# Kernel optimization log

Hardware: AMD Instinct MI355X
Metric: run time of the kernel (lower is better)

Reference implementation:

```python
import jax, jax.numpy as jnp
import numpy as np

EPS = 1e-5
HEADS, DK, DV, FMAP = 8, 32, 64, 32


def _bn(x, gamma, beta, mean, var):
    # inference-mode BatchNorm2d over channel dim of (b, c, h, w)
    inv = gamma / jnp.sqrt(var + EPS)
    return x * inv[None, :, None, None] + (beta - mean * inv)[None, :, None, None]


def setup_inputs() -> dict:
    key = jax.random.key(0)
    ks = jax.random.split(key, 24)
    B, C = 8, 256
    idk, idv = DK * HEADS, DV * HEADS  # 256, 512
    inp = {}
    inp['x'] = jax.random.normal(ks[0], (B, C, FMAP, FMAP), jnp.float32)
    inp['wq'] = jax.random.normal(ks[1], (idk, C), jnp.float32) * (C ** -0.5)
    inp['qgam'] = jax.random.uniform(ks[2], (idk,), jnp.float32, 0.5, 1.5)
    inp['qbet'] = jax.random.normal(ks[3], (idk,), jnp.float32) * 0.1
    inp['qmu'] = jax.random.normal(ks[4], (idk,), jnp.float32) * 0.1
    inp['qvar'] = jax.random.uniform(ks[5], (idk,), jnp.float32, 0.5, 1.5)
    inp['wk'] = jax.random.normal(ks[6], (idk, C), jnp.float32) * (C ** -0.5)
    inp['kgam'] = jax.random.uniform(ks[7], (idk,), jnp.float32, 0.5, 1.5)
    inp['kbet'] = jax.random.normal(ks[8], (idk,), jnp.float32) * 0.1
    inp['kmu'] = jax.random.normal(ks[9], (idk,), jnp.float32) * 0.1
    inp['kvar'] = jax.random.uniform(ks[10], (idk,), jnp.float32, 0.5, 1.5)
    inp['wv'] = jax.random.normal(ks[11], (idv, C), jnp.float32) * (C ** -0.5)
    inp['vgam'] = jax.random.uniform(ks[12], (idv,), jnp.float32, 0.5, 1.5)
    inp['vbet'] = jax.random.normal(ks[13], (idv,), jnp.float32) * 0.1
    inp['vmu'] = jax.random.normal(ks[14], (idv,), jnp.float32) * 0.1
    inp['vvar'] = jax.random.uniform(ks[15], (idv,), jnp.float32, 0.5, 1.5)
    inp['wo'] = jax.random.normal(ks[16], (C, idv), jnp.float32) * (idv ** -0.5)
    inp['bo'] = jax.random.normal(ks[17], (C,), jnp.float32) * 0.1
    inp['ogam'] = jax.random.uniform(ks[18], (C,), jnp.float32, 0.5, 1.5)
    inp['obet'] = jax.random.normal(ks[19], (C,), jnp.float32) * 0.1
    inp['omu'] = jax.random.normal(ks[20], (C,), jnp.float32) * 0.1
    inp['ovar'] = jax.random.uniform(ks[21], (C,), jnp.float32, 0.5, 1.5)
    inp['pos_emb'] = jax.random.normal(ks[22], (FMAP * FMAP, HEADS), jnp.float32) * 0.02
    # deterministic relative-position index buffer, exactly as in the module
    r = np.arange(FMAP)
    pos = np.stack(np.meshgrid(r, r, indexing='ij'), axis=-1).reshape(-1, 2)  # (n, 2)
    rel = np.abs(pos[:, None, :] - pos[None, :, :])  # (n, n, 2)
    inp['pos_indices'] = jnp.asarray(rel[..., 0] * FMAP + rel[..., 1], jnp.int32)
    return inp


def reference(x, wq, qgam, qbet, qmu, qvar, wk, kgam, kbet, kmu, kvar,
              wv, vgam, vbet, vmu, vvar, wo, bo, ogam, obet, omu, ovar,
              pos_emb, pos_indices):
    scale = DK ** -0.5
    B = x.shape[0]
    Fh = Fw = FMAP
    n = Fh * Fw

    def proj(w, g, be, m, v):
        y = jnp.einsum('oc,bchw->bohw', w, x)  # 1x1 conv, no bias
        return _bn(y, g, be, m, v)

    q = proj(wq, qgam, qbet, qmu, qvar)   # (b, H*DK, F, F)
    k = proj(wk, kgam, kbet, kmu, kvar)   # (b, H*DK, F, F)
    v = proj(wv, vgam, vbet, vmu, vvar)   # (b, H*DV, F, F)

    # b (h d) x y -> b h n d
    q = q.reshape(B, HEADS, DK, n).transpose(0, 1, 3, 2)
    k = k.reshape(B, HEADS, DK, n).transpose(0, 1, 3, 2)
    v = v.reshape(B, HEADS, DV, n).transpose(0, 1, 3, 2)

    dots = jnp.einsum('bhid,bhjd->bhij', q, k) * scale  # (b, h, n, n)
    bias = pos_emb[pos_indices]                          # (n, n, h)
    dots = dots + bias.transpose(2, 0, 1)[None] / scale

    attn = jax.nn.softmax(dots, axis=-1)
    out = jnp.einsum('bhij,bhjd->bhid', attn, v)         # (b, h, n, DV)
    out = out.transpose(0, 1, 3, 2).reshape(B, HEADS * DV, Fh, Fw)

    out = jax.nn.gelu(out, approximate=False)
    out = jnp.einsum('oc,bchw->bohw', wo, out) + bo[None, :, None, None]
    return _bn(out, ogam, obet, omu, ovar)
```

## Files before the change

kernel.cpp:

```cpp
#include <hip/hip_runtime.h>
#include <math.h>

#define NB 8
#define NHEADS 8
#define NDK 32
#define NDV 64
#define NSEQ 1024
#define NCIN 256

typedef __attribute__((ext_vector_type(8))) short bf16x8;
typedef __attribute__((ext_vector_type(4))) float f32x4;
typedef __attribute__((ext_vector_type(16))) float f32x16;

#define MFMA16(A, B, C) __builtin_amdgcn_mfma_f32_16x16x32_bf16(A, B, C, 0, 0, 0)
#define MFMA32(A, B, C) __builtin_amdgcn_mfma_f32_32x32x16_bf16(A, B, C, 0, 0, 0)

#define SC2 0.2550347873f
#define PE2 8.1611156f

__device__ __forceinline__ short f2bf(float f) {
    union { float f; unsigned u; } v; v.f = f;
    unsigned r = v.u + 0x7FFFu + ((v.u >> 16) & 1u);
    return (short)(r >> 16);
}

__device__ __forceinline__ unsigned cvt_pk_bf16(float lo, float hi) {
    unsigned r;
    asm("v_cvt_pk_bf16_f32 %0, %1, %2" : "=v"(r) : "v"(lo), "v"(hi));
    return r;
}

__device__ __forceinline__ void gload16(const short* g, short* l) {
    __builtin_amdgcn_global_load_lds(
        (const __attribute__((address_space(1))) void*)g,
        (__attribute__((address_space(3))) void*)l, 16, 0, 0);
}

__global__ __launch_bounds__(256) void prep_trans_kernel(
    const float* __restrict__ x, short* __restrict__ Xt,
    const float* __restrict__ wq, const float* __restrict__ qg, const float* __restrict__ qb,
    const float* __restrict__ qm, const float* __restrict__ qv,
    const float* __restrict__ wk, const float* __restrict__ kg, const float* __restrict__ kb,
    const float* __restrict__ km, const float* __restrict__ kv,
    const float* __restrict__ wv, const float* __restrict__ vg, const float* __restrict__ vb,
    const float* __restrict__ vm, const float* __restrict__ vv,
    const float* __restrict__ wo,
    short* __restrict__ Wqkv, float* __restrict__ Bqkv, short* __restrict__ Wo)
{
    __shared__ float tile[64][65];
    int bid = blockIdx.x, t = threadIdx.x;
    if (bid < 512) {
        int p0 = (bid & 15) * 64, c0 = ((bid >> 4) & 3) * 64, b = bid >> 6;
        int tp = t & 63, tr = t >> 6;
        const float* xb = x + ((size_t)b * NCIN + c0) * NSEQ + p0;
#pragma unroll
        for (int i = 0; i < 16; ++i) {
            int cl = tr * 16 + i;
            tile[cl][tp] = xb[(size_t)cl * NSEQ + tp];
        }
        __syncthreads();
        short* xt = Xt + ((size_t)b * NSEQ + p0) * NCIN + c0;
#pragma unroll
        for (int i = 0; i < 16; ++i) {
            int pl = tr * 16 + i;
            xt[(size_t)pl * NCIN + tp] = f2bf(tile[tp][pl]);
        }
    } else {
        int row = bid - 512;
        if (row < 1024) {
            const float *w, *g, *be, *mu, *va; int o; float sc;
            if (row < 256)      { w = wq; o = row;       g = qg; be = qb; mu = qm; va = qv; sc = SC2; }
            else if (row < 512) { w = wk; o = row - 256; g = kg; be = kb; mu = km; va = kv; sc = 1.f; }
            else                { w = wv; o = row - 512; g = vg; be = vb; mu = vm; va = vv; sc = 1.f; }
            float inv = g[o] * rsqrtf(va[o] + 1e-5f) * sc;
            Wqkv[row * NCIN + t] = f2bf(w[o * NCIN + t] * inv);
            if (t == 0) Bqkv[row] = (be[o] - mu[o] * (g[o] * rsqrtf(va[o] + 1e-5f))) * sc;
        } else {
            int o = row - 1024;
            Wo[o * 512 + t]       = f2bf(wo[o * 512 + t]);
            Wo[o * 512 + 256 + t] = f2bf(wo[o * 512 + 256 + t]);
        }
    }
}

__global__ __launch_bounds__(256) void qkv_gemm(
    const short* __restrict__ Xt, const short* __restrict__ Wqkv, const float* __restrict__ Bqkv,
    short* __restrict__ Qo, short* __restrict__ Ko, short* __restrict__ Vto)
{
    __shared__ short At[128][32];
    __shared__ short Bt[128][32];
    int b = blockIdx.z, p0 = blockIdx.x * 128, o0 = blockIdx.y * 128;
    int t = threadIdx.x, wave = t >> 6, lane = t & 63;
    int wr = wave >> 1, wc = wave & 1, lr = lane & 15, lg = lane >> 4;

    const short* Abase = Xt + ((size_t)b * NSEQ + p0) * NCIN;
    const short* Bbase = Wqkv + (size_t)o0 * NCIN;

    int srow = lane >> 2, scol = (lane & 3) * 8;
    int r0 = (wave * 2) * 16 + srow, r1 = (wave * 2 + 1) * 16 + srow;
    short* lA0 = &At[0][0] + (wave * 2) * 512;
    short* lA1 = &At[0][0] + (wave * 2 + 1) * 512;
    short* lB0 = &Bt[0][0] + (wave * 2) * 512;
    short* lB1 = &Bt[0][0] + (wave * 2 + 1) * 512;

    f32x4 acc[4][4];
#pragma unroll
    for (int m = 0; m < 4; ++m)
#pragma unroll
        for (int n = 0; n < 4; ++n) acc[m][n] = (f32x4){0.f, 0.f, 0.f, 0.f};

    for (int k0 = 0; k0 < NCIN; k0 += 32) {
        gload16(Abase + (size_t)r0 * NCIN + k0 + scol, lA0);
        gload16(Abase + (size_t)r1 * NCIN + k0 + scol, lA1);
        gload16(Bbase + (size_t)r0 * NCIN + k0 + scol, lB0);
        gload16(Bbase + (size_t)r1 * NCIN + k0 + scol, lB1);
        __syncthreads();
        bf16x8 af[4], bfr[4];
#pragma unroll
        for (int m = 0; m < 4; ++m) af[m] = *(const bf16x8*)&At[wr * 64 + m * 16 + lr][lg * 8];
#pragma unroll
        for (int n = 0; n < 4; ++n) bfr[n] = *(const bf16x8*)&Bt[wc * 64 + n * 16 + lr][lg * 8];
#pragma unroll
        for (int m = 0; m < 4; ++m)
#pragma unroll
            for (int n = 0; n < 4; ++n)
                acc[m][n] = MFMA16(af[m], bfr[n], acc[m][n]);
        __syncthreads();
    }

#pragma unroll
    for (int n = 0; n < 4; ++n) {
        int o = o0 + wc * 64 + n * 16 + lr;
        float bias = Bqkv[o];
#pragma unroll
        for (int m = 0; m < 4; ++m) {
            int pr = p0 + wr * 64 + m * 16 + lg * 4;
#pragma unroll
            for (int r = 0; r < 4; ++r) {
                float y = acc[m][n][r] + bias;
                short vv = f2bf(y);
                int p = pr + r;
                if (o < 256) {
                    int hh = o >> 5, d = o & 31;
                    Qo[(((size_t)b * NHEADS + hh) * NSEQ + p) * NDK + d] = vv;
                } else if (o < 512) {
                    int oo = o - 256, hh = oo >> 5, d = oo & 31;
                    Ko[(((size_t)b * NHEADS + hh) * NSEQ + p) * NDK + d] = vv;
                } else {
                    int oo = o - 512, hh = oo >> 6, d = oo & 63;
                    Vto[(((size_t)b * NHEADS + hh) * NDV + d) * NSEQ + p] = vv;
                }
            }
        }
    }
}

__global__ __launch_bounds__(256) void attn_kernel(
    const short* __restrict__ Q, const short* __restrict__ K, const short* __restrict__ Vt,
    const float* __restrict__ pos_emb, short* __restrict__ Xg)
{
    __shared__ float peR[32][64];
    __shared__ short Klds[2][64][36];
    __shared__ short Vlds[2][64][68];
    __shared__ short tb[4][32][68];

    int bid = blockIdx.x;
    int h = bid & 7;
    int qt = (bid >> 3) & 7;
    int b = bid >> 6;
    int t = threadIdx.x, wave = t >> 6, l = t & 63, ql = l & 31, hi = l >> 5;

    {
        int dr = t >> 3, y0 = (t & 7) * 8;
#pragma unroll
        for (int k = 0; k < 8; ++k) {
            int y = y0 + k;
            if (y < 63) {
                int d = 31 - y; d = d < 0 ? -d : d;
                peR[dr][y] = pos_emb[(dr * 32 + d) * NHEADS + h] * PE2;
            }
        }
    }

    size_t bh = (size_t)b * NHEADS + h;
    const short* Qb = Q + bh * NSEQ * NDK;
    const short* Kb = K + bh * NSEQ * NDK;
    const short* Vb = Vt + bh * NDV * NSEQ;

    int q0 = qt * 128 + wave * 32;
    int iq = q0 + ql;
    int qr = iq >> 5;
    int pebase = 31 - ql + 4 * hi;

    bf16x8 qf0 = *(const bf16x8*)(Qb + (size_t)iq * NDK + hi * 8);
    bf16x8 qf1 = *(const bf16x8*)(Qb + (size_t)iq * NDK + 16 + hi * 8);

    int krow = t >> 2, kcol = (t & 3) * 8;
    int vrow = t >> 3, vcol = (t & 7) * 8;

    {
        int4 kreg  = *(const int4*)(Kb + (size_t)krow * NDK + kcol);
        int4 vreg0 = *(const int4*)(Vb + (size_t)vrow * NSEQ + vcol);
        int4 vreg1 = *(const int4*)(Vb + (size_t)(vrow + 32) * NSEQ + vcol);
        *(int4*)&Klds[0][krow][kcol] = kreg;
        *(int4*)&Vlds[0][vrow][vcol] = vreg0;
        *(int4*)&Vlds[0][vrow + 32][vcol] = vreg1;
    }
    __syncthreads();

    float lsum = 0.f;
    f32x16 O0, O1;
#pragma unroll
    for (int r = 0; r < 16; ++r) { O0[r] = 0.f; O1[r] = 0.f; }

    int cur = 0;
    for (int jt = 0; jt < 16; ++jt) {
        int4 kreg, vreg0, vreg1;
        if (jt < 15) {
            int j0n = (jt + 1) * 64;
            kreg  = *(const int4*)(Kb + (size_t)(j0n + krow) * NDK + kcol);
            vreg0 = *(const int4*)(Vb + (size_t)vrow * NSEQ + j0n + vcol);
            vreg1 = *(const int4*)(Vb + (size_t)(vrow + 32) * NSEQ + j0n + vcol);
        }

#pragma unroll
        for (int s = 0; s < 2; ++s) {
            int jr = (jt * 64 + s * 32) >> 5;
            int drb = qr - jr; drb = drb < 0 ? -drb : drb;
            const float* per = &peR[drb][pebase];

            bf16x8 kf0 = *(const bf16x8*)&Klds[cur][s * 32 + ql][hi * 8];
            bf16x8 kf1 = *(const bf16x8*)&Klds[cur][s * 32 + ql][16 + hi * 8];

            f32x16 S;
#pragma unroll
            for (int a = 0; a < 4; ++a)
#pragma unroll
                for (int u = 0; u < 4; ++u)
                    S[4 * a + u] = per[8 * a + u];
            S = MFMA32(kf0, qf0, S);
            S = MFMA32(kf1, qf1, S);

            bf16x8 vf[4];
#pragma unroll
            for (int dn = 0; dn < 2; ++dn)
#pragma unroll
                for (int ks = 0; ks < 2; ++ks)
                    vf[dn * 2 + ks] = *(const bf16x8*)&Vlds[cur][dn * 32 + ql][s * 32 + ks * 16 + hi * 8];

#pragma unroll
            for (int r = 0; r < 16; ++r) S[r] = __builtin_amdgcn_exp2f(S[r]);

            {
                float a0 = S[0] + S[1],   a1 = S[2] + S[3];
                float a2 = S[4] + S[5],   a3 = S[6] + S[7];
                float a4 = S[8] + S[9],   a5 = S[10] + S[11];
                float a6 = S[12] + S[13], a7 = S[14] + S[15];
                float b0 = a0 + a1, b1 = a2 + a3, b2 = a4 + a5, b3 = a6 + a7;
                lsum += (b0 + b1) + (b2 + b3);
            }

            unsigned pk[4][2];
#pragma unroll
            for (int a = 0; a < 4; ++a)
#pragma unroll
                for (int u = 0; u < 2; ++u)
                    pk[a][u] = cvt_pk_bf16(S[4 * a + 2 * u], S[4 * a + 2 * u + 1]);

#pragma unroll
            for (int ks = 0; ks < 2; ++ks) {
                unsigned u0 = pk[2 * ks][0], u2 = pk[2 * ks + 1][0];
                unsigned u1 = pk[2 * ks][1], u3 = pk[2 * ks + 1][1];
                asm("v_permlane32_swap_b32 %0, %1" : "+v"(u0), "+v"(u2));
                asm("v_permlane32_swap_b32 %0, %1" : "+v"(u1), "+v"(u3));
                union { bf16x8 v; unsigned u[4]; } pf;
                pf.u[0] = u0; pf.u[1] = u1; pf.u[2] = u2; pf.u[3] = u3;
                O0 = MFMA32(vf[ks], pf.v, O0);
                O1 = MFMA32(vf[2 + ks], pf.v, O1);
            }
        }

        if (jt < 15) {
            *(int4*)&Klds[cur ^ 1][krow][kcol] = kreg;
            *(int4*)&Vlds[cur ^ 1][vrow][vcol] = vreg0;
            *(int4*)&Vlds[cur ^ 1][vrow + 32][vcol] = vreg1;
            __syncthreads();
            cur ^= 1;
        }
    }

    lsum += __shfl_xor(lsum, 32);
    float inv = 1.0f / lsum;

    short (*tw)[68] = tb[wave];
#pragma unroll
    for (int dn = 0; dn < 2; ++dn)
#pragma unroll
        for (int a = 0; a < 4; ++a) {
            short4 w;
#pragma unroll
            for (int bb = 0; bb < 4; ++bb) {
                float v = (dn ? O1[4 * a + bb] : O0[4 * a + bb]) * inv;
                v = 0.5f * v * (1.f + erff(v * 0.70710678118654752f));
                ((short*)&w)[bb] = f2bf(v);
            }
            *(short4*)&tw[ql][dn * 32 + 8 * a + 4 * hi] = w;
        }
#pragma unroll
    for (int c = 0; c < 4; ++c) {
        int4 val = *(const int4*)&tw[ql][(hi * 4 + c) * 8];
        *(int4*)(Xg + ((size_t)b * NSEQ + q0 + ql) * 512 + h * 64 + (hi * 4 + c) * 8) = val;
    }
}

__global__ __launch_bounds__(256) void out_gemm(
    const short* __restrict__ Xg, const short* __restrict__ Wo,
    const float* __restrict__ bo, const float* __restrict__ og, const float* __restrict__ ob,
    const float* __restrict__ om, const float* __restrict__ ov,
    float* __restrict__ out)
{
    __shared__ short At[128][32];
    __shared__ short Bt[64][32];
    int mt = blockIdx.x, nt = blockIdx.y;
    int t = threadIdx.x, wave = t >> 6, lane = t & 63;
    int wr = wave >> 1, wc = wave & 1, lr = lane & 15, lg = lane >> 4;
    int row0 = mt * 128, o0 = nt * 64;

    int srow = lane >> 2, scol = (lane & 3) * 8;
    int rA0 = (wave * 2) * 16 + srow, rA1 = (wave * 2 + 1) * 16 + srow;
    int rB  = wave * 16 + srow;
    short* lA0 = &At[0][0] + (wave * 2) * 512;
    short* lA1 = &At[0][0] + (wave * 2 + 1) * 512;
    short* lB  = &Bt[0][0] + wave * 512;

    f32x4 acc[4][2];
#pragma unroll
    for (int m = 0; m < 4; ++m)
#pragma unroll
        for (int n = 0; n < 2; ++n) acc[m][n] = (f32x4){0.f, 0.f, 0.f, 0.f};

    for (int k0 = 0; k0 < 512; k0 += 32) {
        gload16(Xg + (size_t)(row0 + rA0) * 512 + k0 + scol, lA0);
        gload16(Xg + (size_t)(row0 + rA1) * 512 + k0 + scol, lA1);
        gload16(Wo + (size_t)(o0 + rB) * 512 + k0 + scol, lB);
        __syncthreads();
        bf16x8 af[4], bfr[2];
#pragma unroll
        for (int m = 0; m < 4; ++m) af[m] = *(const bf16x8*)&At[wr * 64 + m * 16 + lr][lg * 8];
#pragma unroll
        for (int n = 0; n < 2; ++n) bfr[n] = *(const bf16x8*)&Bt[wc * 32 + n * 16 + lr][lg * 8];
#pragma unroll
        for (int m = 0; m < 4; ++m)
#pragma unroll
            for (int n = 0; n < 2; ++n)
                acc[m][n] = MFMA16(af[m], bfr[n], acc[m][n]);
        __syncthreads();
    }

    int b = row0 >> 10;
    int pbase = row0 & 1023;
#pragma unroll
    for (int n = 0; n < 2; ++n) {
        int o = o0 + wc * 32 + n * 16 + lr;
        float inv = og[o] * rsqrtf(ov[o] + 1e-5f);
        float off = bo[o] * inv + ob[o] - om[o] * inv;
        float* dst = out + ((size_t)b * 256 + o) * 1024 + pbase;
#pragma unroll
        for (int m = 0; m < 4; ++m)
#pragma unroll
            for (int r = 0; r < 4; ++r) {
                int p = wr * 64 + m * 16 + lg * 4 + r;
                dst[p] = acc[m][n][r] * inv + off;
            }
    }
}

extern "C" void kernel_launch(void* const* d_in, const int* in_sizes, int n_in,
                              void* d_out, int out_size, void* d_ws, size_t ws_size,
                              hipStream_t stream) {
    const float* x     = (const float*)d_in[0];
    const float* wq    = (const float*)d_in[1];
    const float* qgam  = (const float*)d_in[2];
    const float* qbet  = (const float*)d_in[3];
    const float* qmu   = (const float*)d_in[4];
    const float* qvar  = (const float*)d_in[5];
    const float* wk    = (const float*)d_in[6];
    const float* kgam  = (const float*)d_in[7];
    const float* kbet  = (const float*)d_in[8];
    const float* kmu   = (const float*)d_in[9];
    const float* kvar  = (const float*)d_in[10];
    const float* wv    = (const float*)d_in[11];
    const float* vgam  = (const float*)d_in[12];
    const float* vbet  = (const float*)d_in[13];
    const float* vmu   = (const float*)d_in[14];
    const float* vvar  = (const float*)d_in[15];
    const float* wo    = (const float*)d_in[16];
    const float* bo    = (const float*)d_in[17];
    const float* ogam  = (const float*)d_in[18];
    const float* obet  = (const float*)d_in[19];
    const float* omu   = (const float*)d_in[20];
    const float* ovar  = (const float*)d_in[21];
    const float* pos_emb = (const float*)d_in[22];

    char* ws = (char*)d_ws;
    short* Wqkv = (short*)(ws + 0);
    float* Bqkv = (float*)(ws + 524288);
    short* Wo   = (short*)(ws + 528384);
    short* Xt   = (short*)(ws + 790528);
    short* Qd   = (short*)(ws + 4984832);
    short* Kd   = (short*)(ws + 9179136);
    short* Vtd  = (short*)(ws + 13373440);
    short* Xg   = (short*)(ws + 21762048);

    prep_trans_kernel<<<1792, 256, 0, stream>>>(x, Xt,
                                                wq, qgam, qbet, qmu, qvar,
                                                wk, kgam, kbet, kmu, kvar,
                                                wv, vgam, vbet, vmu, vvar,
                                                wo, Wqkv, Bqkv, Wo);
    qkv_gemm<<<dim3(8, 8, NB), 256, 0, stream>>>(Xt, Wqkv, Bqkv, Qd, Kd, Vtd);
    attn_kernel<<<512, 256, 0, stream>>>(Qd, Kd, Vtd, pos_emb, Xg);
    out_gemm<<<dim3(64, 4), 256, 0, stream>>>(Xg, Wo, bo, ogam, obet, omu, ovar, (float*)d_out);
}
```

Baseline: 73.09 us.

## Prefetch K/V two tiles ahead with unrolled double-buffer and setprio

The attention loop is restructured to unroll by two tiles with fixed LDS buffer indices. Global loads for K/V now run two tiles ahead in two register sets, so each global load has more time to land before it is stored to LDS. The compute phases are wrapped in s_setprio to favour MFMA waves. The cost is more live registers, which could reduce occupancy.

Measured after the change: 71.93 us. No clear change (-1.6%).

```diff
diff --git a/kernel.cpp b/kernel.cpp
--- a/kernel.cpp
+++ b/kernel.cpp
@@ -198,39 +198,20 @@
     int krow = t >> 2, kcol = (t & 3) * 8;
     int vrow = t >> 3, vcol = (t & 7) * 8;
 
-    {
-        int4 kreg  = *(const int4*)(Kb + (size_t)krow * NDK + kcol);
-        int4 vreg0 = *(const int4*)(Vb + (size_t)vrow * NSEQ + vcol);
-        int4 vreg1 = *(const int4*)(Vb + (size_t)(vrow + 32) * NSEQ + vcol);
-        *(int4*)&Klds[0][krow][kcol] = kreg;
-        *(int4*)&Vlds[0][vrow][vcol] = vreg0;
-        *(int4*)&Vlds[0][vrow + 32][vcol] = vreg1;
-    }
-    __syncthreads();
-
     float lsum = 0.f;
     f32x16 O0, O1;
 #pragma unroll
     for (int r = 0; r < 16; ++r) { O0[r] = 0.f; O1[r] = 0.f; }
 
-    int cur = 0;
-    for (int jt = 0; jt < 16; ++jt) {
-        int4 kreg, vreg0, vreg1;
-        if (jt < 15) {
-            int j0n = (jt + 1) * 64;
-            kreg  = *(const int4*)(Kb + (size_t)(j0n + krow) * NDK + kcol);
-            vreg0 = *(const int4*)(Vb + (size_t)vrow * NSEQ + j0n + vcol);
-            vreg1 = *(const int4*)(Vb + (size_t)(vrow + 32) * NSEQ + j0n + vcol);
-        }
-
+    auto compute_tile = [&](int buf, int jt_) {
 #pragma unroll
         for (int s = 0; s < 2; ++s) {
-            int jr = (jt * 64 + s * 32) >> 5;
+            int jr = jt_ * 2 + s;
             int drb = qr - jr; drb = drb < 0 ? -drb : drb;
             const float* per = &peR[drb][pebase];
 
-            bf16x8 kf0 = *(const bf16x8*)&Klds[cur][s * 32 + ql][hi * 8];
-            bf16x8 kf1 = *(const bf16x8*)&Klds[cur][s * 32 + ql][16 + hi * 8];
+            bf16x8 kf0 = *(const bf16x8*)&Klds[buf][s * 32 + ql][hi * 8];
+            bf16x8 kf1 = *(const bf16x8*)&Klds[buf][s * 32 + ql][16 + hi * 8];
 
             f32x16 S;
 #pragma unroll
@@ -246,7 +227,7 @@
             for (int dn = 0; dn < 2; ++dn)
 #pragma unroll
                 for (int ks = 0; ks < 2; ++ks)
-                    vf[dn * 2 + ks] = *(const bf16x8*)&Vlds[cur][dn * 32 + ql][s * 32 + ks * 16 + hi * 8];
+                    vf[dn * 2 + ks] = *(const bf16x8*)&Vlds[buf][dn * 32 + ql][s * 32 + ks * 16 + hi * 8];
 
 #pragma unroll
             for (int r = 0; r < 16; ++r) S[r] = __builtin_amdgcn_exp2f(S[r]);
@@ -279,13 +260,51 @@
                 O1 = MFMA32(vf[2 + ks], pf.v, O1);
             }
         }
-
-        if (jt < 15) {
-            *(int4*)&Klds[cur ^ 1][krow][kcol] = kreg;
-            *(int4*)&Vlds[cur ^ 1][vrow][vcol] = vreg0;
-            *(int4*)&Vlds[cur ^ 1][vrow + 32][vcol] = vreg1;
+    };
+
+    int4 ka, va0, va1, kb2, vb0, vb1;
+    {
+        ka  = *(const int4*)(Kb + (size_t)krow * NDK + kcol);
+        va0 = *(const int4*)(Vb + (size_t)vrow * NSEQ + vcol);
+        va1 = *(const int4*)(Vb + (size_t)(vrow + 32) * NSEQ + vcol);
+        *(int4*)&Klds[0][krow][kcol] = ka;
+        *(int4*)&Vlds[0][vrow][vcol] = va0;
+        *(int4*)&Vlds[0][vrow + 32][vcol] = va1;
+        ka  = *(const int4*)(Kb + (size_t)(64 + krow) * NDK + kcol);
+        va0 = *(const int4*)(Vb + (size_t)vrow * NSEQ + 64 + vcol);
+        va1 = *(const int4*)(Vb + (size_t)(vrow + 32) * NSEQ + 64 + vcol);
+    }
+    __syncthreads();
+
+    for (int jt = 0; jt < 16; jt += 2) {
+        if (jt + 2 < 16) {
+            int j0n = (jt + 2) * 64;
+            kb2 = *(const int4*)(Kb + (size_t)(j0n + krow) * NDK + kcol);
+            vb0 = *(const int4*)(Vb + (size_t)vrow * NSEQ + j0n + vcol);
+            vb1 = *(const int4*)(Vb + (size_t)(vrow + 32) * NSEQ + j0n + vcol);
+        }
+        __builtin_amdgcn_s_setprio(1);
+        compute_tile(0, jt);
+        __builtin_amdgcn_s_setprio(0);
+        *(int4*)&Klds[1][krow][kcol] = ka;
+        *(int4*)&Vlds[1][vrow][vcol] = va0;
+        *(int4*)&Vlds[1][vrow + 32][vcol] = va1;
+        __syncthreads();
+
+        if (jt + 3 < 16) {
+            int j0n = (jt + 3) * 64;
+            ka  = *(const int4*)(Kb + (size_t)(j0n + krow) * NDK + kcol);
+            va0 = *(const int4*)(Vb + (size_t)vrow * NSEQ + j0n + vcol);
+            va1 = *(const int4*)(Vb + (size_t)(vrow + 32) * NSEQ + j0n + vcol);
+        }
+        __builtin_amdgcn_s_setprio(1);
+        compute_tile(1, jt + 1);
+        __builtin_amdgcn_s_setprio(0);
+        if (jt + 2 < 16) {
+            *(int4*)&Klds[0][krow][kcol] = kb2;
+            *(int4*)&Vlds[0][vrow][vcol] = vb0;
+            *(int4*)&Vlds[0][vrow + 32][vcol] = vb1;
             __syncthreads();
-            cur ^= 1;
         }
     }
 
```
